# Kernel optimization log

Measured on AMD Instinct MI355X. Metric: run time of the kernel, lower is better.

## Reference

```python
import jax, jax.numpy as jnp
import numpy as np

T, S, N, E, H, FF = 1024, 2048, 4, 1024, 16, 4096
HD = E // H
EPS = 1e-5


def layer_norm(x, g, b):
    mu = jnp.mean(x, axis=-1, keepdims=True)
    var = jnp.mean(jnp.square(x - mu), axis=-1, keepdims=True)
    return (x - mu) / jnp.sqrt(var + EPS) * g + b


def mha(q_in, k_in, v_in, w_in, b_in, w_out, b_out):
    # q_in: (T,N,E), k_in/v_in: (S,N,E); matches torch F.linear with (3E,E) weight
    t, n, e = q_in.shape
    s = k_in.shape[0]
    wq, wk, wv = jnp.split(w_in, 3, axis=0)
    bq, bk, bv = jnp.split(b_in, 3)
    q = (q_in @ wq.T + bq) * (HD ** -0.5)
    k = k_in @ wk.T + bk
    v = v_in @ wv.T + bv
    # (L,N,E) -> (N*H, L, HD)
    q = q.reshape(t, n * H, HD).transpose(1, 0, 2)
    k = k.reshape(s, n * H, HD).transpose(1, 0, 2)
    v = v.reshape(s, n * H, HD).transpose(1, 0, 2)
    attn = jax.nn.softmax(jnp.einsum('bth,bsh->bts', q, k), axis=-1)
    out = jnp.einsum('bts,bsh->bth', attn, v)  # (N*H, T, HD)
    out = out.transpose(1, 0, 2).reshape(t, n, e)
    return out @ w_out.T + b_out


def setup_inputs() -> dict:
    key = jax.random.key(0)
    ks = jax.random.split(key, 16)
    p = lambda k, shape: jax.random.normal(k, shape, dtype=jnp.float32) * 0.02
    return {
        'tgt': jax.random.normal(ks[0], (T, N, E), dtype=jnp.float32),
        'memory': jax.random.normal(ks[1], (S, N, E), dtype=jnp.float32),
        'sa_w_in': p(ks[2], (3 * E, E)), 'sa_b_in': jnp.zeros((3 * E,), jnp.float32),
        'sa_w_out': p(ks[3], (E, E)), 'sa_b_out': jnp.zeros((E,), jnp.float32),
        'ca_w_in': p(ks[4], (3 * E, E)), 'ca_b_in': jnp.zeros((3 * E,), jnp.float32),
        'ca_w_out': p(ks[5], (E, E)), 'ca_b_out': jnp.zeros((E,), jnp.float32),
        'w1': p(ks[6], (FF, E)), 'b1': jnp.zeros((FF,), jnp.float32),
        'w2': p(ks[7], (E, FF)), 'b2': jnp.zeros((E,), jnp.float32),
        'ln1_g': jnp.ones((E,), jnp.float32), 'ln1_b': jnp.zeros((E,), jnp.float32),
        'ln2_g': jnp.ones((E,), jnp.float32), 'ln2_b': jnp.zeros((E,), jnp.float32),
        'ln3_g': jnp.ones((E,), jnp.float32), 'ln3_b': jnp.zeros((E,), jnp.float32),
    }


def reference(tgt, memory, sa_w_in, sa_b_in, sa_w_out, sa_b_out,
              ca_w_in, ca_b_in, ca_w_out, ca_b_out,
              w1, b1, w2, b2, ln1_g, ln1_b, ln2_g, ln2_b, ln3_g, ln3_b):
    # self-attention block (post-LN residual); dropout = identity (eval mode)
    tgt2 = mha(tgt, tgt, tgt, sa_w_in, sa_b_in, sa_w_out, sa_b_out)
    x = layer_norm(tgt + tgt2, ln1_g, ln1_b)
    # cross-attention block
    tgt2 = mha(x, memory, memory, ca_w_in, ca_b_in, ca_w_out, ca_b_out)
    x = layer_norm(x + tgt2, ln2_g, ln2_b)
    # FFN with relu
    tgt2 = jax.nn.relu(x @ w1.T + b1) @ w2.T + b2
    return layer_norm(x + tgt2, ln3_g, ln3_b)
```

## Files before the change

kernel.cpp:

```cpp
#include <hip/hip_runtime.h>


typedef __bf16 bf16x8 __attribute__((ext_vector_type(8)));
typedef float  f32x4  __attribute__((ext_vector_type(4)));
typedef float  f32x16 __attribute__((ext_vector_type(16)));

#define T_  1024
#define S_  2048
#define NB_ 4
#define E_  1024
#define H_  16
#define HD_ 64
#define FF_ 4096
#define M1_ (T_*NB_)
#define M2_ (S_*NB_)
#define LOG2E 1.44269504088896f

__device__ __forceinline__ unsigned short f2bf(float f){
  unsigned int u = __builtin_bit_cast(unsigned int, f);
  u += 0x7fffu + ((u>>16)&1u);
  return (unsigned short)(u>>16);
}
__device__ __forceinline__ float bf2f(unsigned short h){
  unsigned int u = ((unsigned int)h)<<16;
  return __builtin_bit_cast(float, u);
}

__device__ __forceinline__ void gload16(unsigned short* l, const unsigned short* g){
  __builtin_amdgcn_global_load_lds(
      (const __attribute__((address_space(1))) unsigned int*)g,
      (__attribute__((address_space(3))) unsigned int*)l, 16, 0, 0);
}

__device__ __forceinline__ void perm32swap(unsigned &a, unsigned &b){
  asm("v_permlane32_swap_b32 %0, %1" : "+v"(a), "+v"(b));
}

__device__ __forceinline__ int loff(int row, int kc){
  return ((row>>1)<<6) + (((((row&1)<<2)|kc) ^ ((row>>1)&7))<<3);
}

struct CvtSeg { const float* s; unsigned short* d; int n4; };
struct CvtArgs { CvtSeg seg[8]; int blk_end[8]; };
__global__ __launch_bounds__(256) void f2b_multi_k(CvtArgs a){
  const int b = blockIdx.x;
  int si = 0;
  #pragma unroll
  for (int i=0;i<8;i++) if (b >= a.blk_end[i]) si = i+1;
  const int base = si ? a.blk_end[si-1] : 0;
  const int i4 = (b - base)*256 + threadIdx.x;
  if (i4 >= a.seg[si].n4) return;
  float4 f = ((const float4*)a.seg[si].s)[i4];
  union { unsigned short u[4]; uint2 v; } t;
  t.u[0]=f2bf(f.x); t.u[1]=f2bf(f.y); t.u[2]=f2bf(f.z); t.u[3]=f2bf(f.w);
  ((uint2*)a.seg[si].d)[i4] = t.v;
}

template<int FLAGS, int EPI>
__global__ __launch_bounds__(512, 2) void gemm8_k(
    const unsigned short* __restrict__ A, int lda,
    const unsigned short* __restrict__ B, int ldb,
    const float* __restrict__ bias,
    unsigned short* __restrict__ Cb,
    unsigned short* __restrict__ qb, unsigned short* __restrict__ kb,
    unsigned short* __restrict__ vtb,
    const float* __restrict__ res,
    float* __restrict__ P0, float* __restrict__ P1f,
    float* __restrict__ P2, float* __restrict__ P3,
    int M, int N, int K,
    int nq, int nk, int Lq, int Lkv, float qscale)
{
  __shared__ unsigned short smem[2][4][256*32];
  const int tid  = threadIdx.x;
  const int wave = tid>>6, lane = tid&63;
  const int l15 = lane&15, l4 = lane>>4;

  int bid = blockIdx.x;
  if ((gridDim.x & 7) == 0){ const int cpx = gridDim.x>>3; bid = (bid&7)*cpx + (bid>>3); }
  const int nbm = M>>8;
  const int bm = bid % nbm, bn = bid / nbm;
  const int brow = bm<<8, bcol = bn<<8;
  const int wm0 = (wave>>2)*128, wn = (wave&3)*64;
  const int z   = (EPI==2) ? (int)blockIdx.z : 0;
  const int kh  = (EPI==2) ? (K / (int)gridDim.z) : K;
  const int kbeg = z * kh;
  const int NT  = kh>>5;

  int ldsl[2]; const unsigned short* pA[2]; const unsigned short* pB[2];
  #pragma unroll
  for (int i=0;i<2;i++){
    const int l = i*512 + wave*64 + lane;
    const int grp = l>>3, sl = (l&7) ^ (grp&7);
    const int row = (grp<<1)|(sl>>2), c = sl&3;
    ldsl[i] = l<<3;
    pA[i] = A + (size_t)(brow + row)*lda + kbeg + (c<<3);
    pB[i] = B + (size_t)(bcol + row)*ldb + kbeg + (c<<3);
  }

  f32x4 acc[8][4] = {};

  auto stageA = [&](int t){
    unsigned short* s = smem[0][t&3];
    #pragma unroll
    for (int i=0;i<2;i++) gload16(&s[ldsl[i]], pA[i] + t*32);
  };
  auto stageB = [&](int t){
    unsigned short* s = smem[1][t&3];
    #pragma unroll
    for (int i=0;i<2;i++) gload16(&s[ldsl[i]], pB[i] + t*32);
  };

  stageA(0); stageB(0); stageA(1); stageB(1); stageA(2); stageB(2);
  asm volatile("s_waitcnt vmcnt(8)" ::: "memory");
  __builtin_amdgcn_s_barrier();

  for (int t=0; t<NT; ++t){
    const unsigned short* as = smem[0][t&3];
    const unsigned short* bs = smem[1][t&3];
    const bool pre = (t+3 < NT);

    if (pre) stageA(t+3);
    bf16x8 bf[4], af[4];
    #pragma unroll
    for (int n=0;n<4;n++) bf[n] = *(const bf16x8*)&bs[loff(wn + n*16 + l15, l4)];
    #pragma unroll
    for (int m=0;m<4;m++) af[m] = *(const bf16x8*)&as[loff(wm0 + m*16 + l15, l4)];
    __builtin_amdgcn_s_barrier();
    __builtin_amdgcn_s_setprio(1);
    #pragma unroll
    for (int m=0;m<4;m++)
      #pragma unroll
      for (int n=0;n<4;n++)
        acc[m][n] = __builtin_amdgcn_mfma_f32_16x16x32_bf16(af[m], bf[n], acc[m][n], 0,0,0);
    __builtin_amdgcn_s_setprio(0);
    __builtin_amdgcn_s_barrier();

    if (pre) stageB(t+3);
    #pragma unroll
    for (int m=0;m<4;m++) af[m] = *(const bf16x8*)&as[loff(wm0 + 64 + m*16 + l15, l4)];
    __builtin_amdgcn_s_barrier();
    __builtin_amdgcn_s_setprio(1);
    #pragma unroll
    for (int m=0;m<4;m++)
      #pragma unroll
      for (int n=0;n<4;n++)
        acc[4+m][n] = __builtin_amdgcn_mfma_f32_16x16x32_bf16(af[m], bf[n], acc[4+m][n], 0,0,0);
    __builtin_amdgcn_s_setprio(0);
    if (pre)            asm volatile("s_waitcnt vmcnt(8)" ::: "memory");
    else if (t+2 < NT)  asm volatile("s_waitcnt vmcnt(4)" ::: "memory");
    else                asm volatile("s_waitcnt vmcnt(0)" ::: "memory");
    __builtin_amdgcn_s_barrier();
  }

  if constexpr (EPI == 0){
    #pragma unroll
    for (int mi=0;mi<8;mi++){
      #pragma unroll
      for (int r=0;r<4;r++){
        const int rr = brow + wm0 + mi*16 + l4*4 + r;
        #pragma unroll
        for (int n=0;n<4;n++){
          const int cc = bcol + wn + n*16 + l15;
          float v = acc[mi][n][r] + bias[cc];
          if (FLAGS & 1) v = fmaxf(v, 0.f);
          Cb[(size_t)rr*N + cc] = f2bf(v);
        }
      }
    }
  } else if constexpr (EPI == 1){
    const int voff = nq + nk;
    if (bcol < voff){
      const bool isq = (bcol < nq);
      unsigned short* dst = isq ? qb : kb;
      const int  base  = isq ? 0 : nq;
      const int  L     = isq ? Lq : Lkv;
      const float scale = isq ? qscale : 1.0f;
      #pragma unroll
      for (int mi=0;mi<8;mi++){
        #pragma unroll
        for (int r=0;r<4;r++){
          const int rr = brow + wm0 + mi*16 + l4*4 + r;
          const int t = rr>>2, nn = rr&3;
          #pragma unroll
          for (int n=0;n<4;n++){
            const int cc = bcol + wn + n*16 + l15;
            const int e = cc - base, h = e>>6, d = e&63;
            dst[((size_t)(nn*H_ + h)*L + t)*HD_ + d] = f2bf((acc[mi][n][r] + bias[cc])*scale);
          }
        }
      }
    } else {
      unsigned short* cT = &smem[0][0][0];
      #pragma unroll
      for (int mi=0;mi<8;mi++){
        const int tl = (wm0>>2) + mi*4 + l4;
        #pragma unroll
        for (int n=0;n<4;n++){
          const int ccl = wn + n*16 + l15;
          const float bi = bias[bcol + ccl];
          #pragma unroll
          for (int r=0;r<4;r++){
            const int unit = r*8 + (tl>>3);
            cT[ccl*256 + ((unit ^ (ccl&7))<<3) + (tl&7)] = f2bf(acc[mi][n][r] + bi);
          }
        }
      }
      __syncthreads();
      const int t0 = brow>>2;
      #pragma unroll
      for (int i=0;i<16;i++){
        const int ch = i*512 + tid;
        const int tl8 = ch&7, nn = (ch>>3)&3, ccl = ch>>5;
        const int e = bcol - voff + ccl, h = e>>6, d = e&63;
        const int unit = (nn<<3) | tl8;
        const uint4 v = *(const uint4*)&cT[ccl*256 + ((unit ^ (ccl&7))<<3)];
        *(uint4*)(vtb + ((size_t)(nn*H_ + h)*HD_ + d)*Lkv + t0 + tl8*8) = v;
      }
    }
  } else {
    float* out = (z==0) ? P0 : (z==1) ? P1f : (z==2) ? P2 : P3;
    #pragma unroll
    for (int mi=0;mi<8;mi++){
      #pragma unroll
      for (int r=0;r<4;r++){
        const int rr = brow + wm0 + mi*16 + l4*4 + r;
        #pragma unroll
        for (int n=0;n<4;n++){
          const int cc = bcol + wn + n*16 + l15;
          float v = acc[mi][n][r];
          if (z == 0) v += bias[cc] + res[(size_t)rr*N + cc];
          out[(size_t)rr*N + cc] = v;
        }
      }
    }
  }
}

template<int BN>
__global__ __launch_bounds__(256) void gemm_splitk_k(
    const unsigned short* __restrict__ A, int lda,
    const unsigned short* __restrict__ B, int ldb,
    const float* __restrict__ bias,
    const float* __restrict__ res,
    float* __restrict__ P0, float* __restrict__ P1,
    int M, int N, int K)
{
  constexpr int NW = BN/32;
  __shared__ unsigned short a_sh[128*64];
  __shared__ unsigned short b_sh[BN*64];
  const int tid  = threadIdx.x;
  const int wave = tid>>6;
  const int lane = tid&63;
  const int l15 = lane&15, l4 = lane>>4;
  const int row0 = blockIdx.x*128, col0 = blockIdx.y*BN;
  const int wm = (wave>>1)*64, wn = (wave&1)*(BN/2);
  const int z = blockIdx.z;
  const int kh = K>>1;
  const int kbeg = z*kh;

  const int lrow = tid>>3;
  const int scol = ((tid&7) ^ (lrow&7)) << 3;
  const int dst8 = (tid&7) << 3;

  f32x4 acc[4][NW] = {};

  for (int k0=kbeg; k0<kbeg+kh; k0+=64){
    const unsigned short* ga = A + (size_t)(row0+lrow)*lda + k0 + scol;
    const unsigned short* gb = B + (size_t)(col0+lrow)*ldb + k0 + scol;
    #pragma unroll
    for (int i=0;i<4;i++)
      gload16(&a_sh[(lrow + i*32)*64 + dst8], ga + (size_t)(i*32)*lda);
    #pragma unroll
    for (int i=0;i<BN/32;i++)
      gload16(&b_sh[(lrow + i*32)*64 + dst8], gb + (size_t)(i*32)*ldb);
    __syncthreads();
    #pragma unroll
    for (int kk=0;kk<2;kk++){
      const int sw = (((kk<<2)|l4) ^ (l15&7)) << 3;
      bf16x8 af[4], bfr[NW];
      #pragma unroll
      for (int m=0;m<4;m++)  af[m]  = *(const bf16x8*)&a_sh[(wm + m*16 + l15)*64 + sw];
      #pragma unroll
      for (int n=0;n<NW;n++) bfr[n] = *(const bf16x8*)&b_sh[(wn + n*16 + l15)*64 + sw];
      #pragma unroll
      for (int m=0;m<4;m++)
        #pragma unroll
        for (int n=0;n<NW;n++)
          acc[m][n] = __builtin_amdgcn_mfma_f32_16x16x32_bf16(af[m], bfr[n], acc[m][n], 0,0,0);
    }
    __syncthreads();
  }

  float* out = z ? P1 : P0;
  #pragma unroll
  for (int m=0;m<4;m++){
    #pragma unroll
    for (int r=0;r<4;r++){
      const int rr = row0 + wm + m*16 + l4*4 + r;
      #pragma unroll
      for (int n=0;n<NW;n++){
        const int cc = col0 + wn + n*16 + l15;
        float v = acc[m][n][r];
        if (!z) v += bias[cc] + res[(size_t)rr*N + cc];
        out[(size_t)rr*N + cc] = v;
      }
    }
  }
}

template<int BN>
__global__ __launch_bounds__(256) void gemm_scat_k(
    const unsigned short* __restrict__ A, int lda,
    const unsigned short* __restrict__ B, int ldb,
    const float* __restrict__ bias,
    unsigned short* __restrict__ qb, unsigned short* __restrict__ kb,
    unsigned short* __restrict__ vtb,
    int M, int N, int K, int nq, int nk, int Lq, int Lkv, float qscale)
{
  constexpr int NW = BN/32;
  constexpr int SMEM_ELEMS = (BN==128) ? (128*132) : (128*64 + BN*64);
  __shared__ unsigned short smem[SMEM_ELEMS];
  unsigned short* a_sh = smem;
  unsigned short* b_sh = smem + 128*64;
  const int tid  = threadIdx.x;
  const int wave = tid>>6, lane = tid&63;
  const int l15 = lane&15, l4 = lane>>4;
  const int row0 = blockIdx.x*128, col0 = blockIdx.y*BN;
  const int wm = (wave>>1)*64, wn = (wave&1)*(BN/2);

  const int lrow = tid>>3;
  const int scol = ((tid&7) ^ (lrow&7)) << 3;
  const int dst8 = (tid&7) << 3;

  f32x4 acc[4][NW] = {};

  for (int k0=0; k0<K; k0+=64){
    const unsigned short* ga = A + (size_t)(row0+lrow)*lda + k0 + scol;
    const unsigned short* gb = B + (size_t)(col0+lrow)*ldb + k0 + scol;
    #pragma unroll
    for (int i=0;i<4;i++)
      gload16(&a_sh[(lrow + i*32)*64 + dst8], ga + (size_t)(i*32)*lda);
    #pragma unroll
    for (int i=0;i<BN/32;i++)
      gload16(&b_sh[(lrow + i*32)*64 + dst8], gb + (size_t)(i*32)*ldb);
    __syncthreads();
    #pragma unroll
    for (int kk=0;kk<2;kk++){
      const int sw = (((kk<<2)|l4) ^ (l15&7)) << 3;
      bf16x8 af[4], bfr[NW];
      #pragma unroll
      for (int m=0;m<4;m++)  af[m]  = *(const bf16x8*)&a_sh[(wm + m*16 + l15)*64 + sw];
      #pragma unroll
      for (int n=0;n<NW;n++) bfr[n] = *(const bf16x8*)&b_sh[(wn + n*16 + l15)*64 + sw];
      #pragma unroll
      for (int m=0;m<4;m++)
        #pragma unroll
        for (int n=0;n<NW;n++)
          acc[m][n] = __builtin_amdgcn_mfma_f32_16x16x32_bf16(af[m], bfr[n], acc[m][n], 0,0,0);
    }
    __syncthreads();
  }

  if (col0 < nq + nk){
    const bool isq = (col0 < nq);
    unsigned short* dst = isq ? qb : kb;
    const int  base  = isq ? 0 : nq;
    const int  L     = isq ? Lq : Lkv;
    const float scale = isq ? qscale : 1.0f;
    #pragma unroll
    for (int m=0;m<4;m++){
      #pragma unroll
      for (int r=0;r<4;r++){
        const int rr = row0 + wm + m*16 + l4*4 + r;
        const int t = rr>>2, nn = rr&3;
        #pragma unroll
        for (int n=0;n<NW;n++){
          const int cc = col0 + wn + n*16 + l15;
          const int e = cc - base, h = e>>6, d = e&63;
          const float v = (acc[m][n][r] + bias[cc]) * scale;
          dst[((size_t)(nn*H_ + h)*L + t)*HD_ + d] = f2bf(v);
        }
      }
    }
  }
}

template<bool PARTIAL, int NT>
__global__ __launch_bounds__(256,3) void attn_k(
    const unsigned short* __restrict__ qb, const unsigned short* __restrict__ kb,
    const unsigned short* __restrict__ vtb,
    unsigned short* __restrict__ o_out, float* __restrict__ l_out,
    int T, int S)
{
  static_assert((NT & 1) == 0 && NT >= 4, "NT even");
  __shared__ unsigned short k_sh[2][64*64];
  __shared__ unsigned short v_sh[2][64*64];
  __shared__ float bc_sh[4][32];
  const int tid  = threadIdx.x;
  const int wave = tid>>6, lane = tid&63;
  const int l31  = lane&31;
  const int hv   = lane>>5;
  const int bh   = blockIdx.x;
  const int z    = blockIdx.z;
  const int s_begin = z * (NT*64);
  const int q0   = blockIdx.y*128 + wave*32;
  const size_t qbase = (size_t)bh*T*HD_;
  const size_t kbase = (size_t)bh*S*HD_;
  const size_t vbase = (size_t)bh*HD_*S;

  const int strow = tid>>3;
  const int stch  = tid&7;
  const int sc_sw = (stch ^ (strow&7)) << 3;
  const int dst8  = stch<<3;
  const unsigned short* gk0 = kb  + kbase + (size_t)s_begin*HD_;
  const unsigned short* gv0 = vtb + vbase + s_begin;

  auto stageK = [&](int t, int slot){
    const unsigned short* g = gk0 + (size_t)(t*64)*HD_;
    gload16(&k_sh[slot][(strow   )*64 + dst8], g + (size_t)(strow   )*HD_ + sc_sw);
    gload16(&k_sh[slot][(strow+32)*64 + dst8], g + (size_t)(strow+32)*HD_ + sc_sw);
  };
  auto stageV = [&](int t, int slot){
    const unsigned short* g = gv0 + t*64;
    gload16(&v_sh[slot][(strow   )*64 + dst8], g + (size_t)(strow   )*S + sc_sw);
    gload16(&v_sh[slot][(strow+32)*64 + dst8], g + (size_t)(strow+32)*S + sc_sw);
  };

  bf16x8 qf[4];
  #pragma unroll
  for (int p=0;p<4;p++)
    qf[p] = *(const bf16x8*)(qb + qbase + (size_t)(q0 + l31)*HD_ + p*16 + hv*8);
  asm volatile("" ::: "memory");

  stageK(0, 0);

  f32x16 o0 = {}, o1 = {};
  float rsa = 0.f, rsb = 0.f;
  bf16x8 paA[4], paB[4];

  auto QK = [&](const unsigned short* ksh, f32x16& s0, f32x16& s1){
    #pragma unroll
    for (int p=0;p<4;p++){
      const int slot = 2*p + hv;
      bf16x8 kf0 = *(const bf16x8*)&ksh[(l31     )*64 + ((slot ^ (l31&7))<<3)];
      bf16x8 kf1 = *(const bf16x8*)&ksh[(l31 + 32)*64 + ((slot ^ (l31&7))<<3)];
      s0 = __builtin_amdgcn_mfma_f32_32x32x16_bf16(kf0, qf[p], s0, 0,0,0);
      s1 = __builtin_amdgcn_mfma_f32_32x32x16_bf16(kf1, qf[p], s1, 0,0,0);
    }
  };
  auto PV = [&](const unsigned short* vsh, const bf16x8* pa){
    #pragma unroll
    for (int ks=0;ks<4;ks++){
      const int slot = 2*ks + hv;
      bf16x8 vf0 = *(const bf16x8*)&vsh[(l31     )*64 + ((slot ^ (l31&7))<<3)];
      bf16x8 vf1 = *(const bf16x8*)&vsh[(l31 + 32)*64 + ((slot ^ (l31&7))<<3)];
      o0 = __builtin_amdgcn_mfma_f32_32x32x16_bf16(pa[ks], vf0, o0, 0,0,0);
      o1 = __builtin_amdgcn_mfma_f32_32x32x16_bf16(pa[ks], vf1, o1, 0,0,0);
    }
  };
  auto SM = [&](f32x16& s0, f32x16& s1, bf16x8* pa){
    #pragma unroll
    for (int r=0;r<16;r++){
      s0[r] = __builtin_amdgcn_exp2f(s0[r]);
      s1[r] = __builtin_amdgcn_exp2f(s1[r]);
    }
    #pragma unroll
    for (int r=0;r<16;r+=2){
      rsa += s0[r]   + s1[r];
      rsb += s0[r+1] + s1[r+1];
    }
    #pragma unroll
    for (int ks=0;ks<4;ks++){
      const int base = 8*(ks&1);
      unsigned pkA0, pkA1, pkB0, pkB1;
      if (ks < 2){
        asm("v_cvt_pk_bf16_f32 %0, %1, %2" : "=v"(pkA0) : "v"(s0[base+0]), "v"(s0[base+1]));
        asm("v_cvt_pk_bf16_f32 %0, %1, %2" : "=v"(pkA1) : "v"(s0[base+2]), "v"(s0[base+3]));
        asm("v_cvt_pk_bf16_f32 %0, %1, %2" : "=v"(pkB0) : "v"(s0[base+4]), "v"(s0[base+5]));
        asm("v_cvt_pk_bf16_f32 %0, %1, %2" : "=v"(pkB1) : "v"(s0[base+6]), "v"(s0[base+7]));
      } else {
        asm("v_cvt_pk_bf16_f32 %0, %1, %2" : "=v"(pkA0) : "v"(s1[base+0]), "v"(s1[base+1]));
        asm("v_cvt_pk_bf16_f32 %0, %1, %2" : "=v"(pkA1) : "v"(s1[base+2]), "v"(s1[base+3]));
        asm("v_cvt_pk_bf16_f32 %0, %1, %2" : "=v"(pkB0) : "v"(s1[base+4]), "v"(s1[base+5]));
        asm("v_cvt_pk_bf16_f32 %0, %1, %2" : "=v"(pkB1) : "v"(s1[base+6]), "v"(s1[base+7]));
      }
      perm32swap(pkA0, pkB0);
      perm32swap(pkA1, pkB1);
      union { unsigned w[4]; bf16x8 v; } u;
      u.w[0] = pkA0; u.w[1] = pkA1; u.w[2] = pkB0; u.w[3] = pkB1;
      pa[ks] = u.v;
    }
  };

  {
    stageK(1, 1);
    stageV(0, 0);
    asm volatile("s_waitcnt vmcnt(4)" ::: "memory");
    __builtin_amdgcn_s_barrier();
    f32x16 s0 = {}, s1 = {};
    __builtin_amdgcn_s_setprio(1);
    QK(k_sh[0], s0, s1);
    __builtin_amdgcn_s_setprio(0);
    SM(s0, s1, paA);
    __builtin_amdgcn_s_barrier();
  }

  auto BODY = [&](int i, const bf16x8* paPrev, bf16x8* paCur){
    const int kt = (i+1 < NT) ? (i+1) : (NT-1);
    stageK(kt, (i+1)&1);
    stageV(i, i&1);
    asm volatile("s_waitcnt vmcnt(4)" ::: "memory");
    __builtin_amdgcn_s_barrier();
    f32x16 s0 = {}, s1 = {};
    __builtin_amdgcn_s_setprio(1);
    QK(k_sh[i&1], s0, s1);
    PV(v_sh[(i+1)&1], paPrev);
    __builtin_amdgcn_s_setprio(0);
    SM(s0, s1, paCur);
    __builtin_amdgcn_s_barrier();
  };

  for (int ii=1; ii+1<NT; ii+=2){
    BODY(ii,   paA, paB);
    BODY(ii+1, paB, paA);
  }
  BODY(NT-1, paA, paB);

  asm volatile("s_waitcnt vmcnt(0)" ::: "memory");
  __builtin_amdgcn_s_barrier();
  __builtin_amdgcn_s_setprio(1);
  PV(v_sh[(NT-1)&1], paB);
  __builtin_amdgcn_s_setprio(0);

  float l_run = rsa + rsb;
  {
    unsigned a_ = __builtin_bit_cast(unsigned, l_run), b_ = a_;
    perm32swap(a_, b_);
    l_run += __builtin_bit_cast(float, hv ? a_ : b_);
  }

  if constexpr (PARTIAL){
    const size_t obase = (size_t)(z*64 + bh)*T;
    #pragma unroll
    for (int r=0;r<16;r++){
      const int qr = (r&3) + 8*(r>>2) + 4*hv;
      unsigned short* op = o_out + (obase + q0 + qr)*HD_;
      op[l31]      = f2bf(o0[r]);
      op[l31 + 32] = f2bf(o1[r]);
    }
    if (hv == 0) l_out[obase + q0 + l31] = l_run;
  } else {
    bc_sh[wave][l31] = 1.f / l_run;
    const int nb = bh>>4, hh = bh&15;
    #pragma unroll
    for (int r=0;r<16;r++){
      const int qr  = (r&3) + 8*(r>>2) + 4*hv;
      const float inv = bc_sh[wave][qr];
      const int t = q0 + qr;
      unsigned short* op = o_out + ((size_t)t*NB_ + nb)*E_ + hh*HD_;
      op[l31]      = f2bf(o0[r]*inv);
      op[l31 + 32] = f2bf(o1[r]*inv);
    }
  }
}

__global__ __launch_bounds__(256) void comb_k(
    const unsigned short* __restrict__ opart, const float* __restrict__ lpart,
    unsigned short* __restrict__ outb, int T)
{
  const int bh = blockIdx.y;
  const int t  = blockIdx.x*4 + (threadIdx.x>>6);
  const int d  = threadIdx.x&63;
  const size_t half = (size_t)64*T;
  const size_t row  = (size_t)bh*T + t;
  const float o = bf2f(opart[row*HD_ + d]) + bf2f(opart[(half + row)*HD_ + d]);
  const float l = lpart[row] + lpart[half + row];
  const int nb = bh>>4, hh = bh&15;
  outb[((size_t)t*NB_ + nb)*E_ + hh*HD_ + d] = f2bf(o / l);
}

__global__ __launch_bounds__(256) void ln_k(
    const float* __restrict__ p0, const float* __restrict__ p1,
    const float* __restrict__ p2, const float* __restrict__ p3,
    const float* __restrict__ g, const float* __restrict__ bb,
    float* __restrict__ of, unsigned short* __restrict__ ob)
{
  const int row = blockIdx.x, tid = threadIdx.x;
  const size_t base = (size_t)row*E_;
  float v[4];
  #pragma unroll
  for (int i=0;i<4;i++){
    const int col = tid + 256*i;
    v[i] = p0[base + col] + p1[base + col];
    if (p2) v[i] += p2[base + col];
    if (p3) v[i] += p3[base + col];
  }
  float s  = v[0]+v[1]+v[2]+v[3];
  float s2 = v[0]*v[0]+v[1]*v[1]+v[2]*v[2]+v[3]*v[3];
  #pragma unroll
  for (int off=32; off>0; off>>=1){
    s  += __shfl_down(s, off);
    s2 += __shfl_down(s2, off);
  }
  __shared__ float red[8];
  if ((tid&63)==0){ red[tid>>6] = s; red[4+(tid>>6)] = s2; }
  __syncthreads();
  s  = red[0]+red[1]+red[2]+red[3];
  s2 = red[4]+red[5]+red[6]+red[7];
  const float mu   = s * (1.f/E_);
  const float var  = s2 * (1.f/E_) - mu*mu;
  const float rstd = rsqrtf(var + 1e-5f);
  #pragma unroll
  for (int i=0;i<4;i++){
    const int col = tid + 256*i;
    const float y = (v[i]-mu)*rstd*g[col] + bb[col];
    if (of) of[base + col] = y;
    if (ob) ob[base + col] = f2bf(y);
  }
}

extern "C" void kernel_launch(void* const* d_in, const int* in_sizes, int n_in,
                              void* d_out, int out_size, void* d_ws, size_t ws_size,
                              hipStream_t stream)
{
  const float* tgt      = (const float*)d_in[0];
  const float* mem      = (const float*)d_in[1];
  const float* sa_w_in  = (const float*)d_in[2];
  const float* sa_b_in  = (const float*)d_in[3];
  const float* sa_w_out = (const float*)d_in[4];
  const float* sa_b_out = (const float*)d_in[5];
  const float* ca_w_in  = (const float*)d_in[6];
  const float* ca_b_in  = (const float*)d_in[7];
  const float* ca_w_out = (const float*)d_in[8];
  const float* ca_b_out = (const float*)d_in[9];
  const float* w1 = (const float*)d_in[10];
  const float* b1 = (const float*)d_in[11];
  const float* w2 = (const float*)d_in[12];
  const float* b2 = (const float*)d_in[13];
  const float* ln1_g=(const float*)d_in[14]; const float* ln1_b=(const float*)d_in[15];
  const float* ln2_g=(const float*)d_in[16]; const float* ln2_b=(const float*)d_in[17];
  const float* ln3_g=(const float*)d_in[18]; const float* ln3_b=(const float*)d_in[19];

  char* ws = (char*)d_ws;
  size_t off = 0;
  auto alloc = [&](size_t bytes)->char* {
    char* p = ws + off; off += (bytes + 255) & ~(size_t)255; return p;
  };
  unsigned short* w_sa_in_b  = (unsigned short*)alloc((size_t)3*E_*E_*2);
  unsigned short* w_sa_out_b = (unsigned short*)alloc((size_t)E_*E_*2);
  unsigned short* w_ca_in_b  = (unsigned short*)alloc((size_t)3*E_*E_*2);
  unsigned short* w_ca_out_b = (unsigned short*)alloc((size_t)E_*E_*2);
  unsigned short* w1_b  = (unsigned short*)alloc((size_t)FF_*E_*2);
  unsigned short* w2_b  = (unsigned short*)alloc((size_t)E_*FF_*2);
  unsigned short* tgt_b = (unsigned short*)alloc((size_t)M1_*E_*2);
  unsigned short* mem_b = (unsigned short*)alloc((size_t)M2_*E_*2);
  unsigned short* qbuf  = (unsigned short*)alloc((size_t)64*T_*HD_*2);
  unsigned short* kbuf  = (unsigned short*)alloc((size_t)64*S_*HD_*2);
  unsigned short* vtbuf = (unsigned short*)alloc((size_t)64*S_*HD_*2);
  unsigned short* cbuf  = (unsigned short*)alloc((size_t)M1_*FF_*2);
  unsigned short* atto  = (unsigned short*)alloc((size_t)M1_*E_*2);
  unsigned short* opart = (unsigned short*)alloc((size_t)2*64*T_*HD_*2);
  float*          lpart = (float*)alloc((size_t)2*64*T_*4);
  float* resf = (float*)alloc((size_t)M1_*E_*4);
  float* xf   = (float*)alloc((size_t)M1_*E_*4);
  unsigned short* xb = (unsigned short*)alloc((size_t)M1_*E_*2);
  (void)ws_size; (void)in_sizes; (void)n_in; (void)out_size;

  float* P1 = (float*)opart;
  float* P2 = (float*)kbuf;
  float* P3 = (float*)vtbuf;

  const float QSCALE = 0.125f * LOG2E;

  {
    CvtArgs a;
    const float* srcs[8] = {tgt, mem, sa_w_in, sa_w_out, ca_w_in, ca_w_out, w1, w2};
    unsigned short* dsts[8] = {tgt_b, mem_b, w_sa_in_b, w_sa_out_b, w_ca_in_b, w_ca_out_b, w1_b, w2_b};
    size_t ns[8] = {(size_t)M1_*E_, (size_t)M2_*E_, (size_t)3*E_*E_, (size_t)E_*E_,
                    (size_t)3*E_*E_, (size_t)E_*E_, (size_t)FF_*E_, (size_t)E_*FF_};
    int blk = 0;
    for (int i=0;i<8;i++){
      a.seg[i].s = srcs[i]; a.seg[i].d = dsts[i]; a.seg[i].n4 = (int)(ns[i]/4);
      blk += (a.seg[i].n4 + 255)/256;
      a.blk_end[i] = blk;
    }
    f2b_multi_k<<<blk, 256, 0, stream>>>(a);
  }

  gemm8_k<0,1><<<(M1_/256)*((3*E_)/256), 512, 0, stream>>>(
      tgt_b, E_, w_sa_in_b, E_, sa_b_in, nullptr, qbuf, kbuf, vtbuf,
      nullptr, nullptr, nullptr, nullptr, nullptr,
      M1_, 3*E_, E_, E_, E_, T_, T_, QSCALE);
  attn_k<false,16><<<dim3(64, T_/128, 1), 256, 0, stream>>>(
      qbuf, kbuf, vtbuf, atto, nullptr, T_, T_);
  gemm_splitk_k<64><<<dim3(M1_/128, E_/64, 2), 256, 0, stream>>>(
      atto, E_, w_sa_out_b, E_, sa_b_out, tgt, resf, P1, M1_, E_, E_);
  ln_k<<<M1_, 256, 0, stream>>>(resf, P1, nullptr, nullptr, ln1_g, ln1_b, xf, xb);

  gemm8_k<0,1><<<(M2_/256)*((2*E_)/256), 512, 0, stream>>>(
      mem_b, E_, w_ca_in_b + (size_t)E_*E_, E_, ca_b_in + E_, nullptr,
      nullptr, kbuf, vtbuf,
      nullptr, nullptr, nullptr, nullptr, nullptr,
      M2_, 2*E_, E_, 0, E_, S_, S_, QSCALE);
  gemm_scat_k<64><<<dim3(M1_/128, E_/64), 256, 0, stream>>>(
      xb, E_, w_ca_in_b, E_, ca_b_in, qbuf, nullptr, nullptr,
      M1_, E_, E_, E_, 0, T_, S_, QSCALE);
  attn_k<true,16><<<dim3(64, T_/128, 2), 256, 0, stream>>>(
      qbuf, kbuf, vtbuf, opart, lpart, T_, S_);
  comb_k<<<dim3(T_/4, 64), 256, 0, stream>>>(opart, lpart, atto, T_);
  gemm_splitk_k<64><<<dim3(M1_/128, E_/64, 2), 256, 0, stream>>>(
      atto, E_, w_ca_out_b, E_, ca_b_out, xf, resf, P1, M1_, E_, E_);
  ln_k<<<M1_, 256, 0, stream>>>(resf, P1, nullptr, nullptr, ln2_g, ln2_b, xf, xb);

  gemm8_k<5,0><<<(M1_/256)*(FF_/256), 512, 0, stream>>>(
      xb, E_, w1_b, E_, b1, cbuf, nullptr, nullptr, nullptr,
      nullptr, nullptr, nullptr, nullptr, nullptr,
      M1_, FF_, E_, 0, 0, 0, 0, 0.f);
  gemm8_k<0,2><<<dim3((M1_/256)*(E_/256), 1, 4), 512, 0, stream>>>(
      cbuf, FF_, w2_b, FF_, b2, nullptr, nullptr, nullptr, nullptr,
      xf, resf, P1, P2, P3,
      M1_, E_, FF_, 0, 0, 0, 0, 0.f);
  ln_k<<<M1_, 256, 0, stream>>>(resf, P1, P2, P3, ln3_g, ln3_b, (float*)d_out, nullptr);
}
```

Measured before the change: 406.0 us.

## Double-buffer split-K GEMM and route FFN down-projection through it

```diff
diff --git a/kernel.cpp b/kernel.cpp
--- a/kernel.cpp
+++ b/kernel.cpp
@@ -64,9 +64,6 @@
     unsigned short* __restrict__ Cb,
     unsigned short* __restrict__ qb, unsigned short* __restrict__ kb,
     unsigned short* __restrict__ vtb,
-    const float* __restrict__ res,
-    float* __restrict__ P0, float* __restrict__ P1f,
-    float* __restrict__ P2, float* __restrict__ P3,
     int M, int N, int K,
     int nq, int nk, int Lq, int Lkv, float qscale)
 {
@@ -81,10 +78,7 @@
   const int bm = bid % nbm, bn = bid / nbm;
   const int brow = bm<<8, bcol = bn<<8;
   const int wm0 = (wave>>2)*128, wn = (wave&3)*64;
-  const int z   = (EPI==2) ? (int)blockIdx.z : 0;
-  const int kh  = (EPI==2) ? (K / (int)gridDim.z) : K;
-  const int kbeg = z * kh;
-  const int NT  = kh>>5;
+  const int NT  = K>>5;
 
   int ldsl[2]; const unsigned short* pA[2]; const unsigned short* pB[2];
   #pragma unroll
@@ -93,8 +87,8 @@
     const int grp = l>>3, sl = (l&7) ^ (grp&7);
     const int row = (grp<<1)|(sl>>2), c = sl&3;
     ldsl[i] = l<<3;
-    pA[i] = A + (size_t)(brow + row)*lda + kbeg + (c<<3);
-    pB[i] = B + (size_t)(bcol + row)*ldb + kbeg + (c<<3);
+    pA[i] = A + (size_t)(brow + row)*lda + (c<<3);
+    pB[i] = B + (size_t)(bcol + row)*ldb + (c<<3);
   }
 
   f32x4 acc[8][4] = {};
@@ -167,7 +161,7 @@
         }
       }
     }
-  } else if constexpr (EPI == 1){
+  } else {
     const int voff = nq + nk;
     if (bcol < voff){
       const bool isq = (bcol < nq);
@@ -217,22 +211,6 @@
         *(uint4*)(vtb + ((size_t)(nn*H_ + h)*HD_ + d)*Lkv + t0 + tl8*8) = v;
       }
     }
-  } else {
-    float* out = (z==0) ? P0 : (z==1) ? P1f : (z==2) ? P2 : P3;
-    #pragma unroll
-    for (int mi=0;mi<8;mi++){
-      #pragma unroll
-      for (int r=0;r<4;r++){
-        const int rr = brow + wm0 + mi*16 + l4*4 + r;
-        #pragma unroll
-        for (int n=0;n<4;n++){
-          const int cc = bcol + wn + n*16 + l15;
-          float v = acc[mi][n][r];
-          if (z == 0) v += bias[cc] + res[(size_t)rr*N + cc];
-          out[(size_t)rr*N + cc] = v;
-        }
-      }
-    }
   }
 }
 
@@ -246,8 +224,9 @@
     int M, int N, int K)
 {
   constexpr int NW = BN/32;
-  __shared__ unsigned short a_sh[128*64];
-  __shared__ unsigned short b_sh[BN*64];
+  constexpr int NLD = 4 + BN/32;
+  __shared__ unsigned short a_sh[2][128*64];
+  __shared__ unsigned short b_sh[2][BN*64];
   const int tid  = threadIdx.x;
   const int wave = tid>>6;
   const int lane = tid&63;
@@ -257,39 +236,58 @@
   const int z = blockIdx.z;
   const int kh = K>>1;
   const int kbeg = z*kh;
+  const int NT = kh>>6;
 
   const int lrow = tid>>3;
   const int scol = ((tid&7) ^ (lrow&7)) << 3;
   const int dst8 = (tid&7) << 3;
 
+  auto stage = [&](int t){
+    const unsigned short* ga = A + (size_t)(row0+lrow)*lda + kbeg + t*64 + scol;
+    const unsigned short* gb = B + (size_t)(col0+lrow)*ldb + kbeg + t*64 + scol;
+    unsigned short* as = a_sh[t&1];
+    unsigned short* bs = b_sh[t&1];
+    #pragma unroll
+    for (int i=0;i<4;i++)
+      gload16(&as[(lrow + i*32)*64 + dst8], ga + (size_t)(i*32)*lda);
+    #pragma unroll
+    for (int i=0;i<BN/32;i++)
+      gload16(&bs[(lrow + i*32)*64 + dst8], gb + (size_t)(i*32)*ldb);
+  };
+
   f32x4 acc[4][NW] = {};
 
-  for (int k0=kbeg; k0<kbeg+kh; k0+=64){
-    const unsigned short* ga = A + (size_t)(row0+lrow)*lda + k0 + scol;
-    const unsigned short* gb = B + (size_t)(col0+lrow)*ldb + k0 + scol;
-    #pragma unroll
-    for (int i=0;i<4;i++)
-      gload16(&a_sh[(lrow + i*32)*64 + dst8], ga + (size_t)(i*32)*lda);
-    #pragma unroll
-    for (int i=0;i<BN/32;i++)
-      gload16(&b_sh[(lrow + i*32)*64 + dst8], gb + (size_t)(i*32)*ldb);
-    __syncthreads();
+  stage(0);
+  for (int t=0; t<NT; ++t){
+    if (t+1 < NT){
+      stage(t+1);
+      asm volatile("s_waitcnt vmcnt(" "6" ")" ::: "memory");
+    } else {
+      asm volatile("s_waitcnt vmcnt(0)" ::: "memory");
+    }
+    __builtin_amdgcn_s_barrier();
+
+    const unsigned short* as = a_sh[t&1];
+    const unsigned short* bs = b_sh[t&1];
+    __builtin_amdgcn_s_setprio(1);
     #pragma unroll
     for (int kk=0;kk<2;kk++){
       const int sw = (((kk<<2)|l4) ^ (l15&7)) << 3;
       bf16x8 af[4], bfr[NW];
       #pragma unroll
-      for (int m=0;m<4;m++)  af[m]  = *(const bf16x8*)&a_sh[(wm + m*16 + l15)*64 + sw];
-      #pragma unroll
-      for (int n=0;n<NW;n++) bfr[n] = *(const bf16x8*)&b_sh[(wn + n*16 + l15)*64 + sw];
+      for (int m=0;m<4;m++)  af[m]  = *(const bf16x8*)&as[(wm + m*16 + l15)*64 + sw];
+      #pragma unroll
+      for (int n=0;n<NW;n++) bfr[n] = *(const bf16x8*)&bs[(wn + n*16 + l15)*64 + sw];
       #pragma unroll
       for (int m=0;m<4;m++)
         #pragma unroll
         for (int n=0;n<NW;n++)
           acc[m][n] = __builtin_amdgcn_mfma_f32_16x16x32_bf16(af[m], bfr[n], acc[m][n], 0,0,0);
     }
-    __syncthreads();
-  }
+    __builtin_amdgcn_s_setprio(0);
+    __builtin_amdgcn_s_barrier();
+  }
+  static_assert(NLD == 6 || BN != 64, "vmcnt literal assumes BN=64");
 
   float* out = z ? P1 : P0;
   #pragma unroll
@@ -581,7 +579,6 @@
 
 __global__ __launch_bounds__(256) void ln_k(
     const float* __restrict__ p0, const float* __restrict__ p1,
-    const float* __restrict__ p2, const float* __restrict__ p3,
     const float* __restrict__ g, const float* __restrict__ bb,
     float* __restrict__ of, unsigned short* __restrict__ ob)
 {
@@ -592,8 +589,6 @@
   for (int i=0;i<4;i++){
     const int col = tid + 256*i;
     v[i] = p0[base + col] + p1[base + col];
-    if (p2) v[i] += p2[base + col];
-    if (p3) v[i] += p3[base + col];
   }
   float s  = v[0]+v[1]+v[2]+v[3];
   float s2 = v[0]*v[0]+v[1]*v[1]+v[2]*v[2]+v[3]*v[3];
@@ -667,8 +662,6 @@
   (void)ws_size; (void)in_sizes; (void)n_in; (void)out_size;
 
   float* P1 = (float*)opart;
-  float* P2 = (float*)kbuf;
-  float* P3 = (float*)vtbuf;
 
   const float QSCALE = 0.125f * LOG2E;
 
@@ -689,18 +682,16 @@
 
   gemm8_k<0,1><<<(M1_/256)*((3*E_)/256), 512, 0, stream>>>(
       tgt_b, E_, w_sa_in_b, E_, sa_b_in, nullptr, qbuf, kbuf, vtbuf,
-      nullptr, nullptr, nullptr, nullptr, nullptr,
       M1_, 3*E_, E_, E_, E_, T_, T_, QSCALE);
   attn_k<false,16><<<dim3(64, T_/128, 1), 256, 0, stream>>>(
       qbuf, kbuf, vtbuf, atto, nullptr, T_, T_);
   gemm_splitk_k<64><<<dim3(M1_/128, E_/64, 2), 256, 0, stream>>>(
       atto, E_, w_sa_out_b, E_, sa_b_out, tgt, resf, P1, M1_, E_, E_);
-  ln_k<<<M1_, 256, 0, stream>>>(resf, P1, nullptr, nullptr, ln1_g, ln1_b, xf, xb);
+  ln_k<<<M1_, 256, 0, stream>>>(resf, P1, ln1_g, ln1_b, xf, xb);
 
   gemm8_k<0,1><<<(M2_/256)*((2*E_)/256), 512, 0, stream>>>(
       mem_b, E_, w_ca_in_b + (size_t)E_*E_, E_, ca_b_in + E_, nullptr,
       nullptr, kbuf, vtbuf,
-      nullptr, nullptr, nullptr, nullptr, nullptr,
       M2_, 2*E_, E_, 0, E_, S_, S_, QSCALE);
   gemm_scat_k<64><<<dim3(M1_/128, E_/64), 256, 0, stream>>>(
       xb, E_, w_ca_in_b, E_, ca_b_in, qbuf, nullptr, nullptr,
@@ -710,15 +701,12 @@
   comb_k<<<dim3(T_/4, 64), 256, 0, stream>>>(opart, lpart, atto, T_);
   gemm_splitk_k<64><<<dim3(M1_/128, E_/64, 2), 256, 0, stream>>>(
       atto, E_, w_ca_out_b, E_, ca_b_out, xf, resf, P1, M1_, E_, E_);
-  ln_k<<<M1_, 256, 0, stream>>>(resf, P1, nullptr, nullptr, ln2_g, ln2_b, xf, xb);
+  ln_k<<<M1_, 256, 0, stream>>>(resf, P1, ln2_g, ln2_b, xf, xb);
 
   gemm8_k<5,0><<<(M1_/256)*(FF_/256), 512, 0, stream>>>(
       xb, E_, w1_b, E_, b1, cbuf, nullptr, nullptr, nullptr,
-      nullptr, nullptr, nullptr, nullptr, nullptr,
       M1_, FF_, E_, 0, 0, 0, 0, 0.f);
-  gemm8_k<0,2><<<dim3((M1_/256)*(E_/256), 1, 4), 512, 0, stream>>>(
-      cbuf, FF_, w2_b, FF_, b2, nullptr, nullptr, nullptr, nullptr,
-      xf, resf, P1, P2, P3,
-      M1_, E_, FF_, 0, 0, 0, 0, 0.f);
-  ln_k<<<M1_, 256, 0, stream>>>(resf, P1, P2, P3, ln3_g, ln3_b, (float*)d_out, nullptr);
-}
+  gemm_splitk_k<64><<<dim3(M1_/128, E_/64, 2), 256, 0, stream>>>(
+      cbuf, FF_, w2_b, FF_, b2, xf, resf, P1, M1_, E_, FF_);
+  ln_k<<<M1_, 256, 0, stream>>>(resf, P1, ln3_g, ln3_b, (float*)d_out, nullptr);
+}
```

Result: faster. 380.3 us (-6.3%).
